# Optimization experiments

Hardware: AMD Instinct MI355X
Metric: run time of the kernel (lower is better)

## Reference

```python
import jax, jax.numpy as jnp
import numpy as np

B, S, D = 2, 1024, 1024
H, KV, HD = 16, 4, 64
E, K, F = 8, 2, 2048
EPS = 1e-6
THETA = 10000.0
LAYER = 0


def setup_inputs() -> dict:
    key = jax.random.key(0)
    ks = jax.random.split(key, 12)
    sc = 0.02
    return {
        "hidden_states": jax.random.normal(ks[0], (B, S, D), jnp.float32),
        "position_ids": jnp.broadcast_to(jnp.arange(S, dtype=jnp.int32), (B, S)),
        "gate_scores": jnp.zeros((1, B, S, E), jnp.float32),
        "ln1_w": jnp.ones((D,), jnp.float32),
        "ln2_w": jnp.ones((D,), jnp.float32),
        "wq": jax.random.normal(ks[1], (D, H * HD), jnp.float32) * sc,
        "wk": jax.random.normal(ks[2], (D, KV * HD), jnp.float32) * sc,
        "wv": jax.random.normal(ks[3], (D, KV * HD), jnp.float32) * sc,
        "wo": jax.random.normal(ks[4], (H * HD, D), jnp.float32) * sc,
        "gate_w": jax.random.normal(ks[5], (D, E), jnp.float32) * sc,
        "w1": jax.random.normal(ks[6], (E, D, F), jnp.float32) * sc,
        "w3": jax.random.normal(ks[7], (E, D, F), jnp.float32) * sc,
        "w2": jax.random.normal(ks[8], (E, F, D), jnp.float32) * sc,
    }


def rms_norm(x, w):
    var = jnp.mean(jnp.square(x), axis=-1, keepdims=True)
    return x * jax.lax.rsqrt(var + EPS) * w


def rotate_half(x):
    x1, x2 = jnp.split(x, 2, axis=-1)
    return jnp.concatenate([-x2, x1], axis=-1)


def apply_rope(q, k, position_ids):
    inv_freq = 1.0 / (THETA ** (jnp.arange(0, HD, 2, dtype=jnp.float32) / HD))
    freqs = position_ids.astype(jnp.float32)[..., None] * inv_freq  # [B,S,HD/2]
    emb = jnp.concatenate([freqs, freqs], axis=-1)  # [B,S,HD]
    cos = jnp.cos(emb)[:, :, None, :]
    sin = jnp.sin(emb)[:, :, None, :]
    q = q * cos + rotate_half(q) * sin
    k = k * cos + rotate_half(k) * sin
    return q, k


def attention(x, position_ids, wq, wk, wv, wo):
    q = (x @ wq).reshape(B, S, H, HD)
    k = (x @ wk).reshape(B, S, KV, HD)
    v = (x @ wv).reshape(B, S, KV, HD)
    q, k = apply_rope(q, k, position_ids)
    rep = H // KV
    k = jnp.repeat(k, rep, axis=2)  # [B,S,H,HD]
    v = jnp.repeat(v, rep, axis=2)
    scores = jnp.einsum("bqhd,bkhd->bhqk", q, k) / jnp.sqrt(jnp.float32(HD))
    causal = jnp.tril(jnp.ones((S, S), bool))
    scores = jnp.where(causal, scores, jnp.finfo(scores.dtype).min)
    p = jax.nn.softmax(scores, axis=-1)
    out = jnp.einsum("bhqk,bkhd->bqhd", p, v).reshape(B, S, H * HD)
    return out @ wo


def moe(x, gate_w, w1, w3, w2):
    xt = x.reshape(-1, D)  # [T,D]
    router_logits = xt @ gate_w  # [T,E]
    routing_weights = jax.nn.softmax(router_logits.astype(jnp.float32), axis=-1)
    routing_scores = routing_weights.reshape(B, S, E)
    top_w, top_e = jax.lax.top_k(routing_weights, K)  # [T,K]
    top_w = top_w / jnp.sum(top_w, axis=-1, keepdims=True)
    top_w = top_w.astype(xt.dtype)
    # combined per-(token,expert) weight; zero when not routed
    comb = jnp.sum(jax.nn.one_hot(top_e, E, dtype=xt.dtype) * top_w[..., None], axis=1)  # [T,E]
    # SwiGLU experts, dense-dispatch formulation (same math as gather/scatter)
    h = jax.nn.silu(jnp.einsum("td,edf->etf", xt, w1)) * jnp.einsum("td,edf->etf", xt, w3)
    y = jnp.einsum("etf,efd->etd", h, w2)  # [E,T,D]
    out = jnp.einsum("etd,te->td", y, comb)
    return out.reshape(B, S, D), routing_scores


def reference(hidden_states, position_ids, gate_scores, ln1_w, ln2_w, wq, wk, wv, wo, gate_w, w1, w3, w2):
    residual = hidden_states
    h = rms_norm(hidden_states, ln1_w)
    h = residual + attention(h, position_ids, wq, wk, wv, wo)
    residual = h
    hn = rms_norm(h, ln2_w)
    moe_out, routing_scores = moe(hn, gate_w, w1, w3, w2)
    h = residual + moe_out
    gate_scores = gate_scores.at[LAYER].set(routing_scores)
    return h, gate_scores
```

## Files before the change

kernel.cpp:

```cpp
#include <hip/hip_runtime.h>
#include <hip/hip_bf16.h>
#include <stdint.h>

using bf16 = __hip_bfloat16;
using bf16x8 = __attribute__((ext_vector_type(8))) __bf16;
using f32x4  = __attribute__((ext_vector_type(4))) float;

#define NTOK 2048
#define DIM 1024
#define NH 16
#define NKV 4
#define HDIM 64
#define NE 8
#define NF 2048
#define SEQ 1024
#define MAXR 5120
#define MAXTILES 40

__device__ __forceinline__ float b2f(unsigned short u){ unsigned v=((unsigned)u)<<16; float f; __builtin_memcpy(&f,&v,4); return f; }
__device__ __forceinline__ unsigned short f2b(float f){ bf16 h=__float2bfloat16(f); unsigned short u; __builtin_memcpy(&u,&h,2); return u; }

__global__ void k_zero_i32(int* p, int n){ int i=blockIdx.x*256+threadIdx.x; if(i<n) p[i]=0; }

__global__ __launch_bounds__(256) void k_transpose(const float* __restrict__ in, bf16* __restrict__ out, int R, int C){
  __shared__ float tile[32][33];
  int bx = blockIdx.x*32, by = blockIdx.y*32;
  size_t base = (size_t)blockIdx.z * R * C;
  int x = threadIdx.x, y0 = threadIdx.y;
  const float* src = in + base;
  bf16* dst = out + base;
#pragma unroll
  for (int i=0;i<4;i++){ int r = y0 + i*8; tile[r][x] = src[(size_t)(by+r)*C + bx + x]; }
  __syncthreads();
#pragma unroll
  for (int i=0;i<4;i++){ int c = y0 + i*8; dst[(size_t)(bx+c)*R + by + x] = __float2bfloat16(tile[x][c]); }
}

__global__ __launch_bounds__(256) void k_tbf(const bf16* __restrict__ in, bf16* __restrict__ out, int R, int C){
  __shared__ unsigned short tile[32][33];
  int bx = blockIdx.x*32, by = blockIdx.y*32;
  size_t base = (size_t)blockIdx.z * R * C;
  const unsigned short* src = (const unsigned short*)in + base;
  unsigned short* dst = (unsigned short*)out + base;
  int x = threadIdx.x, y0 = threadIdx.y;
#pragma unroll
  for (int i=0;i<4;i++){ int r = y0 + i*8; tile[r][x] = src[(size_t)(by+r)*C + bx + x]; }
  __syncthreads();
#pragma unroll
  for (int i=0;i<4;i++){ int c = y0 + i*8; dst[(size_t)(bx+c)*R + by + x] = tile[x][c]; }
}

__global__ __launch_bounds__(256) void k_rmsnorm(const float* __restrict__ x, const float* __restrict__ w, bf16* __restrict__ out){
  int row = blockIdx.x, t = threadIdx.x;
  const float4 v = ((const float4*)(x + (size_t)row*DIM))[t];
  float ss = v.x*v.x + v.y*v.y + v.z*v.z + v.w*v.w;
#pragma unroll
  for (int m=1;m<64;m<<=1) ss += __shfl_xor(ss, m);
  __shared__ float red[4];
  if ((t&63)==0) red[t>>6] = ss;
  __syncthreads();
  float tot = red[0]+red[1]+red[2]+red[3];
  float r = rsqrtf(tot * (1.0f/DIM) + 1e-6f);
  const float4 wv = ((const float4*)w)[t];
  ushort4 o;
  o.x = f2b(v.x*r*wv.x); o.y = f2b(v.y*r*wv.y); o.z = f2b(v.z*r*wv.z); o.w = f2b(v.w*r*wv.w);
  ((ushort4*)(out + (size_t)row*DIM))[t] = o;
}

#define BM 128
#define BN 128
#define BK 32

template<int MODE>
__global__ __launch_bounds__(256) void k_gemm(
    const bf16* __restrict__ A, const bf16* __restrict__ Bt,
    bf16* __restrict__ Cb, float* __restrict__ Cf, const float* __restrict__ resid,
    const int* __restrict__ tile_expert, const int* __restrict__ row_tok,
    const float* __restrict__ row_w, const int* __restrict__ row_slot,
    int N, int K)
{
  int tn = blockIdx.x, tm = blockIdx.y;
  int e = 0;
  if constexpr (MODE >= 2){ e = tile_expert[tm]; if (e < 0) return; }
  const bf16* Ablk = A + (size_t)tm*BM*K;
  const bf16* Bblk = Bt + ((MODE>=2) ? (size_t)e*N*K : (size_t)0) + (size_t)tn*BN*K;

  __shared__ bf16 lA[BM*BK];
  __shared__ bf16 lB[BN*BK];

  int t = threadIdx.x;
  int lane = t & 63, wave = t >> 6;
  int wr = wave >> 1, wc = wave & 1;
  int lr = lane & 15, lg = lane >> 4;

  int sr = t >> 2;
  int sk = (t & 3) * 8;

  f32x4 acc[4][4] = {};

  for (int k0 = 0; k0 < K; k0 += BK){
    bf16x8 va0 = *(const bf16x8*)(Ablk + (size_t)sr*K + k0 + sk);
    bf16x8 va1 = *(const bf16x8*)(Ablk + (size_t)(64+sr)*K + k0 + sk);
    bf16x8 vb0 = *(const bf16x8*)(Bblk + (size_t)sr*K + k0 + sk);
    bf16x8 vb1 = *(const bf16x8*)(Bblk + (size_t)(64+sr)*K + k0 + sk);
    __syncthreads();
    *(bf16x8*)(lA + t*8) = va0;
    *(bf16x8*)(lA + 2048 + t*8) = va1;
    *(bf16x8*)(lB + t*8) = vb0;
    *(bf16x8*)(lB + 2048 + t*8) = vb1;
    __syncthreads();
    bf16x8 af[4], bfv[4];
#pragma unroll
    for (int m=0;m<4;m++) af[m]  = *(const bf16x8*)(lA + (wr*64 + m*16 + lr)*BK + lg*8);
#pragma unroll
    for (int n=0;n<4;n++) bfv[n] = *(const bf16x8*)(lB + (wc*64 + n*16 + lr)*BK + lg*8);
#pragma unroll
    for (int m=0;m<4;m++)
#pragma unroll
      for (int n=0;n<4;n++)
        acc[m][n] = __builtin_amdgcn_mfma_f32_16x16x32_bf16(af[m], bfv[n], acc[m][n], 0, 0, 0);
  }

#pragma unroll
  for (int m=0;m<4;m++){
#pragma unroll
    for (int n=0;n<4;n++){
      int col = tn*BN + wc*64 + n*16 + lr;
#pragma unroll
      for (int j=0;j<4;j++){
        int row = tm*BM + wr*64 + m*16 + lg*4 + j;
        float v = acc[m][n][j];
        if constexpr (MODE==0 || MODE==2){
          Cb[(size_t)row*N + col] = __float2bfloat16(v);
        } else if constexpr (MODE==1){
          Cf[(size_t)row*N + col] = v + resid[(size_t)row*N + col];
        } else {
          int tok = row_tok[row];
          if (tok >= 0) Cf[((size_t)row_slot[row]*NTOK + tok)*DIM + col] = v * row_w[row];
        }
      }
    }
  }
}

__global__ __launch_bounds__(64) void k_rope(const bf16* __restrict__ qkv, const int* __restrict__ pos_ids,
    bf16* __restrict__ qr, bf16* __restrict__ kr, bf16* __restrict__ vr){
  int tk = blockIdx.x;
  int b = tk >> 10, s = tk & 1023;
  int d = threadIdx.x;
  float p = (float)pos_ids[tk];
  int i = d & 31;
  float freq = p * powf(10000.0f, -(float)(2*i)*(1.0f/HDIM));
  float sn, cs;
  sincosf(freq, &sn, &cs);
  const bf16* row = qkv + (size_t)tk*1536;
#pragma unroll
  for (int h=0; h<NH; h++){
    float x  = __bfloat162float(row[h*64 + d]);
    float xp = __bfloat162float(row[h*64 + ((d+32)&63)]);
    float rh = (d<32) ? -xp : xp;
    qr[(((size_t)(b*NH+h)*SEQ)+s)*HDIM + d] = __float2bfloat16(x*cs + rh*sn);
  }
#pragma unroll
  for (int h=0; h<NKV; h++){
    float x  = __bfloat162float(row[1024 + h*64 + d]);
    float xp = __bfloat162float(row[1024 + h*64 + ((d+32)&63)]);
    float rh = (d<32) ? -xp : xp;
    kr[(((size_t)(b*NKV+h)*SEQ)+s)*HDIM + d] = __float2bfloat16(x*cs + rh*sn);
    vr[(((size_t)(b*NKV+h)*SEQ)+s)*HDIM + d] = row[1280 + h*64 + d];
  }
}

__global__ __launch_bounds__(64) void k_attn_mfma(const bf16* __restrict__ qr, const bf16* __restrict__ kr,
    const bf16* __restrict__ vT, bf16* __restrict__ out){
  int qt = blockIdx.x, h = blockIdx.y, b = blockIdx.z;
  int lane = threadIdx.x;
  int g = lane >> 4, c = lane & 15;
  int kv = h >> 2;
  int qbase = qt*16;
  const bf16* Qb = qr + (((size_t)(b*NH+h)*SEQ) + qbase)*HDIM;
  const bf16* Kb = kr + ((size_t)(b*NKV+kv)*SEQ)*HDIM;
  const bf16* Vt = vT + ((size_t)(b*NKV+kv)*HDIM)*SEQ;

  bf16x8 qa[2];
  qa[0] = *(const bf16x8*)(Qb + (size_t)c*HDIM + g*8);
  qa[1] = *(const bf16x8*)(Qb + (size_t)c*HDIM + 32 + g*8);

  f32x4 acc[4] = {};
  float m[4], l[4];
#pragma unroll
  for (int j=0;j<4;j++){ m[j] = -1e30f; l[j] = 0.f; }

  __shared__ bf16 P[16][40];

  int kend = qbase + 15;
  for (int k0 = 0; k0 <= kend; k0 += 32){
    f32x4 s[2] = {};
#pragma unroll
    for (int cn=0;cn<2;cn++){
#pragma unroll
      for (int dk=0;dk<2;dk++){
        bf16x8 kb = *(const bf16x8*)(Kb + (size_t)(k0+cn*16+c)*HDIM + dk*32 + g*8);
        s[cn] = __builtin_amdgcn_mfma_f32_16x16x32_bf16(qa[dk], kb, s[cn], 0, 0, 0);
      }
    }
    float sv[2][4];
    bool boundary = (k0 + 31 > qbase);
#pragma unroll
    for (int cn=0;cn<2;cn++){
#pragma unroll
      for (int j=0;j<4;j++){
        float v = s[cn][j] * 0.125f;
        if (boundary){
          int cg = k0 + cn*16 + c, rg = qbase + g*4 + j;
          if (cg > rg) v = -1e30f;
        }
        sv[cn][j] = v;
      }
    }
#pragma unroll
    for (int j=0;j<4;j++){
      float rmax = fmaxf(sv[0][j], sv[1][j]);
#pragma unroll
      for (int mk=1;mk<16;mk<<=1) rmax = fmaxf(rmax, __shfl_xor(rmax, mk));
      float mn = fmaxf(m[j], rmax);
      float corr = __expf(m[j] - mn);
      m[j] = mn;
      float p0 = __expf(sv[0][j] - mn);
      float p1 = __expf(sv[1][j] - mn);
      float rs = p0 + p1;
#pragma unroll
      for (int mk=1;mk<16;mk<<=1) rs += __shfl_xor(rs, mk);
      l[j] = l[j]*corr + rs;
#pragma unroll
      for (int db=0;db<4;db++) acc[db][j] *= corr;
      P[g*4+j][c]      = __float2bfloat16(p0);
      P[g*4+j][16+c]   = __float2bfloat16(p1);
    }
    __syncthreads();
    bf16x8 pa = *(const bf16x8*)(&P[c][g*8]);
#pragma unroll
    for (int db=0;db<4;db++){
      bf16x8 vb = *(const bf16x8*)(Vt + (size_t)(db*16+c)*SEQ + k0 + g*8);
      acc[db] = __builtin_amdgcn_mfma_f32_16x16x32_bf16(pa, vb, acc[db], 0, 0, 0);
    }
    __syncthreads();
  }
#pragma unroll
  for (int j=0;j<4;j++){
    float inv = 1.f / l[j];
    size_t rowoff = (size_t)(b*SEQ + qbase + g*4 + j)*1024 + h*64;
#pragma unroll
    for (int db=0;db<4;db++)
      out[rowoff + db*16 + c] = __float2bfloat16(acc[db][j] * inv);
  }
}

__global__ __launch_bounds__(64) void k_router(const float* __restrict__ h1, const float* __restrict__ ln2w,
    const float* __restrict__ gw, float* __restrict__ scores,
    int* __restrict__ top_e, float* __restrict__ top_w, int* __restrict__ cnt){
  int tk = blockIdx.x, lane = threadIdx.x;
  const float* xr = h1 + (size_t)tk*DIM;
  const float4* x4 = (const float4*)xr;
  float4 xv[4];
  float ss = 0.f;
#pragma unroll
  for (int i=0;i<4;i++){
    xv[i] = x4[lane*4+i];
    ss += xv[i].x*xv[i].x + xv[i].y*xv[i].y + xv[i].z*xv[i].z + xv[i].w*xv[i].w;
  }
#pragma unroll
  for (int mm=1;mm<64;mm<<=1) ss += __shfl_xor(ss, mm);
  float r = rsqrtf(ss*(1.0f/DIM) + 1e-6f);
  float acc[8] = {0,0,0,0,0,0,0,0};
#pragma unroll
  for (int i=0;i<16;i++){
    int d = lane*16 + i;
    float xd = ((const float*)xv)[i];
    float xn = xd * r * ln2w[d];
    const float* g = gw + (size_t)d*NE;
#pragma unroll
    for (int e=0;e<8;e++) acc[e] += xn * g[e];
  }
#pragma unroll
  for (int e=0;e<8;e++){
#pragma unroll
    for (int mm=1;mm<64;mm<<=1) acc[e] += __shfl_xor(acc[e], mm);
  }
  float mx = acc[0];
#pragma unroll
  for (int e=1;e<8;e++) mx = fmaxf(mx, acc[e]);
  float w[8]; float se = 0.f;
#pragma unroll
  for (int e=0;e<8;e++){ w[e] = expf(acc[e]-mx); se += w[e]; }
  float inv = 1.f/se;
#pragma unroll
  for (int e=0;e<8;e++) w[e] *= inv;
  if (lane < 8) scores[(size_t)tk*NE + lane] = w[lane];
  if (lane == 0){
    int e1=0; float m1=w[0];
#pragma unroll
    for (int i=1;i<8;i++) if (w[i] > m1){ m1=w[i]; e1=i; }
    int e2=-1; float m2=-1.f;
#pragma unroll
    for (int i=0;i<8;i++) if (i!=e1 && w[i] > m2){ m2=w[i]; e2=i; }
    float s12 = m1 + m2;
    top_e[2*tk] = e1;   top_w[2*tk]   = m1/s12;
    top_e[2*tk+1] = e2; top_w[2*tk+1] = m2/s12;
    atomicAdd(&cnt[e1], 1); atomicAdd(&cnt[e2], 1);
  }
}

__global__ __launch_bounds__(256) void k_offsets(const int* __restrict__ cnt, int* __restrict__ seg_off,
    int* __restrict__ tile_expert, int* __restrict__ row_tok){
  int t = threadIdx.x;
  for (int i=t;i<MAXR;i+=256) row_tok[i] = -1;
  for (int i=t;i<MAXTILES;i+=256) tile_expert[i] = -1;
  __syncthreads();
  if (t == 0){
    int off = 0;
    for (int e=0;e<NE;e++){
      seg_off[e] = off;
      int nt = (cnt[e] + 127) >> 7;
      for (int i=0;i<nt;i++) tile_expert[(off>>7)+i] = e;
      off += nt << 7;
    }
  }
}

__global__ __launch_bounds__(256) void k_scatter(const int* __restrict__ top_e, const float* __restrict__ top_w,
    const int* __restrict__ seg_off, int* __restrict__ cnt2,
    int* __restrict__ row_tok, float* __restrict__ row_w, int* __restrict__ row_slot){
  int tkn = blockIdx.x*256 + threadIdx.x;
  if (tkn >= NTOK) return;
#pragma unroll
  for (int k=0;k<2;k++){
    int e = top_e[2*tkn+k];
    int p = atomicAdd(&cnt2[e], 1);
    int r = seg_off[e] + p;
    row_tok[r] = tkn; row_w[r] = top_w[2*tkn+k]; row_slot[r] = k;
  }
}

__global__ __launch_bounds__(256) void k_gather(const int* __restrict__ row_tok, const bf16* __restrict__ xn,
    bf16* __restrict__ Xg){
  int r = blockIdx.x, t = threadIdx.x;
  int tok = row_tok[r];
  ushort4* dst = (ushort4*)(Xg + (size_t)r*DIM) + t;
  if (tok < 0){ ushort4 z; z.x=0; z.y=0; z.z=0; z.w=0; *dst = z; }
  else *dst = ((const ushort4*)(xn + (size_t)tok*DIM))[t];
}

__global__ __launch_bounds__(256) void k_silumul(const bf16* __restrict__ a, const bf16* __restrict__ b, bf16* __restrict__ o){
  size_t i = (size_t)blockIdx.x*256 + threadIdx.x;
  ushort4 ua = ((const ushort4*)a)[i];
  ushort4 ub = ((const ushort4*)b)[i];
  ushort4 uo;
  { float fa=b2f(ua.x), fb=b2f(ub.x); uo.x = f2b(fa/(1.f+__expf(-fa))*fb); }
  { float fa=b2f(ua.y), fb=b2f(ub.y); uo.y = f2b(fa/(1.f+__expf(-fa))*fb); }
  { float fa=b2f(ua.z), fb=b2f(ub.z); uo.z = f2b(fa/(1.f+__expf(-fa))*fb); }
  { float fa=b2f(ua.w), fb=b2f(ub.w); uo.w = f2b(fa/(1.f+__expf(-fa))*fb); }
  ((ushort4*)o)[i] = uo;
}

__global__ __launch_bounds__(256) void k_final(const float* __restrict__ h1, const float* __restrict__ ybuf, float* __restrict__ out){
  size_t i = (size_t)blockIdx.x*256 + threadIdx.x;
  float4 a  = ((const float4*)h1)[i];
  float4 b0 = ((const float4*)ybuf)[i];
  float4 b1 = ((const float4*)(ybuf + (size_t)NTOK*DIM))[i];
  float4 r;
  r.x = a.x+b0.x+b1.x; r.y = a.y+b0.y+b1.y; r.z = a.z+b0.z+b1.z; r.w = a.w+b0.w+b1.w;
  ((float4*)out)[i] = r;
}

extern "C" void kernel_launch(void* const* d_in, const int* in_sizes, int n_in,
                              void* d_out, int out_size, void* d_ws, size_t ws_size,
                              hipStream_t stream){
  const float* hidden = (const float*)d_in[0];
  const int*   pos    = (const int*)d_in[1];
  const float* ln1    = (const float*)d_in[3];
  const float* ln2    = (const float*)d_in[4];
  const float* wq     = (const float*)d_in[5];
  const float* wk     = (const float*)d_in[6];
  const float* wv     = (const float*)d_in[7];
  const float* wo     = (const float*)d_in[8];
  const float* gw     = (const float*)d_in[9];
  const float* w1     = (const float*)d_in[10];
  const float* w3     = (const float*)d_in[11];
  const float* w2     = (const float*)d_in[12];
  float* out1 = (float*)d_out;
  float* out2 = out1 + (size_t)NTOK*DIM;

  char* p = (char*)d_ws;
  auto take = [&](size_t bytes){ void* r = (void*)p; p += (bytes + 255) & ~(size_t)255; return r; };
  bf16* wqkvT = (bf16*)take((size_t)1536*1024*2);
  bf16* woT   = (bf16*)take((size_t)1024*1024*2);
  bf16* w1T   = (bf16*)take((size_t)NE*NF*DIM*2);
  bf16* w3T   = (bf16*)take((size_t)NE*NF*DIM*2);
  bf16* w2T   = (bf16*)take((size_t)NE*DIM*NF*2);
  float* h1   = (float*)take((size_t)NTOK*DIM*4);
  bf16* xn2   = (bf16*)take((size_t)NTOK*DIM*2);
  int*  cnt   = (int*)take(64);
  int*  cnt2  = cnt + 8;
  int*  seg_off     = (int*)take(64);
  int*  tile_expert = (int*)take(MAXTILES*4);
  int*  top_e  = (int*)take((size_t)NTOK*2*4);
  float* top_w = (float*)take((size_t)NTOK*2*4);
  int*  row_tok  = (int*)take((size_t)MAXR*4);
  float* row_w   = (float*)take((size_t)MAXR*4);
  int*  row_slot = (int*)take((size_t)MAXR*4);
  bf16* Xg    = (bf16*)take((size_t)MAXR*DIM*2);
  bf16* h1buf = (bf16*)take((size_t)MAXR*NF*2);
  bf16* h3buf = (bf16*)take((size_t)MAXR*NF*2);
  bf16* hbuf  = (bf16*)take((size_t)MAXR*NF*2);
  char* ra = (char*)Xg;
  bf16* xn1 = (bf16*)ra;       ra += (size_t)NTOK*DIM*2;
  bf16* qkv = (bf16*)ra;       ra += (size_t)NTOK*1536*2;
  bf16* qr  = (bf16*)ra;       ra += (size_t)NTOK*DIM*2;
  bf16* krp = (bf16*)ra;       ra += (size_t)NTOK*NKV*HDIM*2;
  bf16* vrp = (bf16*)ra;       ra += (size_t)NTOK*NKV*HDIM*2;
  bf16* vTp = (bf16*)ra;       ra += (size_t)NTOK*NKV*HDIM*2;
  bf16* attn_out = (bf16*)ra;  ra += (size_t)NTOK*DIM*2;
  float* ybuf = (float*)h1buf;

  k_zero_i32<<<dim3(1), dim3(256), 0, stream>>>(cnt, 16);
  k_transpose<<<dim3(32,32,1), dim3(32,8), 0, stream>>>(wq, wqkvT, 1024, 1024);
  k_transpose<<<dim3(8,32,1),  dim3(32,8), 0, stream>>>(wk, wqkvT + (size_t)1024*1024, 1024, 256);
  k_transpose<<<dim3(8,32,1),  dim3(32,8), 0, stream>>>(wv, wqkvT + (size_t)1280*1024, 1024, 256);
  k_transpose<<<dim3(32,32,1), dim3(32,8), 0, stream>>>(wo, woT, 1024, 1024);
  k_transpose<<<dim3(NF/32, DIM/32, NE), dim3(32,8), 0, stream>>>(w1, w1T, DIM, NF);
  k_transpose<<<dim3(NF/32, DIM/32, NE), dim3(32,8), 0, stream>>>(w3, w3T, DIM, NF);
  k_transpose<<<dim3(DIM/32, NF/32, NE), dim3(32,8), 0, stream>>>(w2, w2T, NF, DIM);
  k_rmsnorm<<<dim3(NTOK), dim3(256), 0, stream>>>(hidden, ln1, xn1);
  k_gemm<0><<<dim3(1536/BN, NTOK/BM), dim3(256), 0, stream>>>(xn1, wqkvT, qkv, nullptr, nullptr, nullptr, nullptr, nullptr, nullptr, 1536, 1024);
  k_rope<<<dim3(NTOK), dim3(64), 0, stream>>>(qkv, pos, qr, krp, vrp);
  k_tbf<<<dim3(HDIM/32, SEQ/32, 2*NKV), dim3(32,8), 0, stream>>>(vrp, vTp, SEQ, HDIM);
  k_attn_mfma<<<dim3(SEQ/16, NH, 2), dim3(64), 0, stream>>>(qr, krp, vTp, attn_out);
  k_gemm<1><<<dim3(DIM/BN, NTOK/BM), dim3(256), 0, stream>>>(attn_out, woT, nullptr, h1, hidden, nullptr, nullptr, nullptr, nullptr, DIM, 1024);
  k_rmsnorm<<<dim3(NTOK), dim3(256), 0, stream>>>(h1, ln2, xn2);
  k_router<<<dim3(NTOK), dim3(64), 0, stream>>>(h1, ln2, gw, out2, top_e, top_w, cnt);
  k_offsets<<<dim3(1), dim3(256), 0, stream>>>(cnt, seg_off, tile_expert, row_tok);
  k_scatter<<<dim3(NTOK/256), dim3(256), 0, stream>>>(top_e, top_w, seg_off, cnt2, row_tok, row_w, row_slot);
  k_gather<<<dim3(MAXR), dim3(256), 0, stream>>>(row_tok, xn2, Xg);
  k_gemm<2><<<dim3(NF/BN, MAXTILES), dim3(256), 0, stream>>>(Xg, w1T, h1buf, nullptr, nullptr, tile_expert, nullptr, nullptr, nullptr, NF, DIM);
  k_gemm<2><<<dim3(NF/BN, MAXTILES), dim3(256), 0, stream>>>(Xg, w3T, h3buf, nullptr, nullptr, tile_expert, nullptr, nullptr, nullptr, NF, DIM);
  k_silumul<<<dim3((unsigned)((size_t)MAXR*NF/4/256)), dim3(256), 0, stream>>>(h1buf, h3buf, hbuf);
  k_gemm<3><<<dim3(DIM/BN, MAXTILES), dim3(256), 0, stream>>>(hbuf, w2T, nullptr, ybuf, nullptr, tile_expert, row_tok, row_w, row_slot, DIM, NF);
  k_final<<<dim3(NTOK*DIM/4/256), dim3(256), 0, stream>>>(h1, ybuf, out1);
}
```

Baseline: 621.9 us.

## Load GEMM tiles directly to LDS and fuse w1/w3 expert GEMMs

The GEMM staging now uses global_load_lds so tiles go from global memory straight into LDS, skipping the register round-trip, and the per-wave row mapping is changed to match. The w1 and w3 expert weights are transposed into one interleaved buffer per expert so a single grouped GEMM with doubled N produces both projections. The SiLU-multiply kernel reads both halves from each row of that buffer. This saves a launch and one read of the gathered activations, but the direct-to-LDS path needs its layout to line up with the MFMA fragment reads.

```diff
diff --git a/kernel.cpp b/kernel.cpp
--- a/kernel.cpp
+++ b/kernel.cpp
@@ -20,15 +20,21 @@
 __device__ __forceinline__ float b2f(unsigned short u){ unsigned v=((unsigned)u)<<16; float f; __builtin_memcpy(&f,&v,4); return f; }
 __device__ __forceinline__ unsigned short f2b(float f){ bf16 h=__float2bfloat16(f); unsigned short u; __builtin_memcpy(&u,&h,2); return u; }
 
+typedef __attribute__((address_space(3))) unsigned int lds_u32;
+typedef const __attribute__((address_space(1))) unsigned int glb_u32;
+__device__ __forceinline__ void lds16(const void* g, void* l){
+  __builtin_amdgcn_global_load_lds((glb_u32*)g, (lds_u32*)l, 16, 0, 0);
+}
+
 __global__ void k_zero_i32(int* p, int n){ int i=blockIdx.x*256+threadIdx.x; if(i<n) p[i]=0; }
 
-__global__ __launch_bounds__(256) void k_transpose(const float* __restrict__ in, bf16* __restrict__ out, int R, int C){
+__global__ __launch_bounds__(256) void k_transpose(const float* __restrict__ in, bf16* __restrict__ out,
+    int R, int C, size_t inz, size_t outz){
   __shared__ float tile[32][33];
   int bx = blockIdx.x*32, by = blockIdx.y*32;
-  size_t base = (size_t)blockIdx.z * R * C;
+  const float* src = in + (size_t)blockIdx.z * inz;
+  bf16* dst = out + (size_t)blockIdx.z * outz;
   int x = threadIdx.x, y0 = threadIdx.y;
-  const float* src = in + base;
-  bf16* dst = out + base;
 #pragma unroll
   for (int i=0;i<4;i++){ int r = y0 + i*8; tile[r][x] = src[(size_t)(by+r)*C + bx + x]; }
   __syncthreads();
@@ -93,21 +99,17 @@
   int wr = wave >> 1, wc = wave & 1;
   int lr = lane & 15, lg = lane >> 4;
 
-  int sr = t >> 2;
-  int sk = (t & 3) * 8;
+  int srow = wave*32 + (lane >> 2);
+  int scol = (lane & 3) * 8;
 
   f32x4 acc[4][4] = {};
 
   for (int k0 = 0; k0 < K; k0 += BK){
-    bf16x8 va0 = *(const bf16x8*)(Ablk + (size_t)sr*K + k0 + sk);
-    bf16x8 va1 = *(const bf16x8*)(Ablk + (size_t)(64+sr)*K + k0 + sk);
-    bf16x8 vb0 = *(const bf16x8*)(Bblk + (size_t)sr*K + k0 + sk);
-    bf16x8 vb1 = *(const bf16x8*)(Bblk + (size_t)(64+sr)*K + k0 + sk);
     __syncthreads();
-    *(bf16x8*)(lA + t*8) = va0;
-    *(bf16x8*)(lA + 2048 + t*8) = va1;
-    *(bf16x8*)(lB + t*8) = vb0;
-    *(bf16x8*)(lB + 2048 + t*8) = vb1;
+    lds16(Ablk + (size_t)srow*K        + k0 + scol, lA + wave*1024);
+    lds16(Ablk + (size_t)(srow+16)*K   + k0 + scol, lA + wave*1024 + 512);
+    lds16(Bblk + (size_t)srow*K        + k0 + scol, lB + wave*1024);
+    lds16(Bblk + (size_t)(srow+16)*K   + k0 + scol, lB + wave*1024 + 512);
     __syncthreads();
     bf16x8 af[4], bfv[4];
 #pragma unroll
@@ -351,16 +353,19 @@
   else *dst = ((const ushort4*)(xn + (size_t)tok*DIM))[t];
 }
 
-__global__ __launch_bounds__(256) void k_silumul(const bf16* __restrict__ a, const bf16* __restrict__ b, bf16* __restrict__ o){
+__global__ __launch_bounds__(256) void k_silumul(const bf16* __restrict__ h13, bf16* __restrict__ o){
   size_t i = (size_t)blockIdx.x*256 + threadIdx.x;
-  ushort4 ua = ((const ushort4*)a)[i];
-  ushort4 ub = ((const ushort4*)b)[i];
+  size_t r = i >> 9;
+  int fq = (int)(i & 511);
+  const bf16* rowp = h13 + r*(2*NF);
+  ushort4 ua = ((const ushort4*)rowp)[fq];
+  ushort4 ub = ((const ushort4*)(rowp + NF))[fq];
   ushort4 uo;
   { float fa=b2f(ua.x), fb=b2f(ub.x); uo.x = f2b(fa/(1.f+__expf(-fa))*fb); }
   { float fa=b2f(ua.y), fb=b2f(ub.y); uo.y = f2b(fa/(1.f+__expf(-fa))*fb); }
   { float fa=b2f(ua.z), fb=b2f(ub.z); uo.z = f2b(fa/(1.f+__expf(-fa))*fb); }
   { float fa=b2f(ua.w), fb=b2f(ub.w); uo.w = f2b(fa/(1.f+__expf(-fa))*fb); }
-  ((ushort4*)o)[i] = uo;
+  ((ushort4*)(o))[i] = uo;
 }
 
 __global__ __launch_bounds__(256) void k_final(const float* __restrict__ h1, const float* __restrict__ ybuf, float* __restrict__ out){
@@ -395,8 +400,7 @@
   auto take = [&](size_t bytes){ void* r = (void*)p; p += (bytes + 255) & ~(size_t)255; return r; };
   bf16* wqkvT = (bf16*)take((size_t)1536*1024*2);
   bf16* woT   = (bf16*)take((size_t)1024*1024*2);
-  bf16* w1T   = (bf16*)take((size_t)NE*NF*DIM*2);
-  bf16* w3T   = (bf16*)take((size_t)NE*NF*DIM*2);
+  bf16* w13T  = (bf16*)take((size_t)NE*2*NF*DIM*2);
   bf16* w2T   = (bf16*)take((size_t)NE*DIM*NF*2);
   float* h1   = (float*)take((size_t)NTOK*DIM*4);
   bf16* xn2   = (bf16*)take((size_t)NTOK*DIM*2);
@@ -409,10 +413,9 @@
   int*  row_tok  = (int*)take((size_t)MAXR*4);
   float* row_w   = (float*)take((size_t)MAXR*4);
   int*  row_slot = (int*)take((size_t)MAXR*4);
-  bf16* Xg    = (bf16*)take((size_t)MAXR*DIM*2);
-  bf16* h1buf = (bf16*)take((size_t)MAXR*NF*2);
-  bf16* h3buf = (bf16*)take((size_t)MAXR*NF*2);
-  bf16* hbuf  = (bf16*)take((size_t)MAXR*NF*2);
+  bf16* Xg     = (bf16*)take((size_t)MAXR*DIM*2);
+  bf16* h13buf = (bf16*)take((size_t)MAXR*2*NF*2);
+  bf16* hbuf   = (bf16*)take((size_t)MAXR*NF*2);
   char* ra = (char*)Xg;
   bf16* xn1 = (bf16*)ra;       ra += (size_t)NTOK*DIM*2;
   bf16* qkv = (bf16*)ra;       ra += (size_t)NTOK*1536*2;
@@ -421,16 +424,16 @@
   bf16* vrp = (bf16*)ra;       ra += (size_t)NTOK*NKV*HDIM*2;
   bf16* vTp = (bf16*)ra;       ra += (size_t)NTOK*NKV*HDIM*2;
   bf16* attn_out = (bf16*)ra;  ra += (size_t)NTOK*DIM*2;
-  float* ybuf = (float*)h1buf;
+  float* ybuf = (float*)h13buf;
 
   k_zero_i32<<<dim3(1), dim3(256), 0, stream>>>(cnt, 16);
-  k_transpose<<<dim3(32,32,1), dim3(32,8), 0, stream>>>(wq, wqkvT, 1024, 1024);
-  k_transpose<<<dim3(8,32,1),  dim3(32,8), 0, stream>>>(wk, wqkvT + (size_t)1024*1024, 1024, 256);
-  k_transpose<<<dim3(8,32,1),  dim3(32,8), 0, stream>>>(wv, wqkvT + (size_t)1280*1024, 1024, 256);
-  k_transpose<<<dim3(32,32,1), dim3(32,8), 0, stream>>>(wo, woT, 1024, 1024);
-  k_transpose<<<dim3(NF/32, DIM/32, NE), dim3(32,8), 0, stream>>>(w1, w1T, DIM, NF);
-  k_transpose<<<dim3(NF/32, DIM/32, NE), dim3(32,8), 0, stream>>>(w3, w3T, DIM, NF);
-  k_transpose<<<dim3(DIM/32, NF/32, NE), dim3(32,8), 0, stream>>>(w2, w2T, NF, DIM);
+  k_transpose<<<dim3(32,32,1), dim3(32,8), 0, stream>>>(wq, wqkvT, 1024, 1024, (size_t)1024*1024, (size_t)1024*1024);
+  k_transpose<<<dim3(8,32,1),  dim3(32,8), 0, stream>>>(wk, wqkvT + (size_t)1024*1024, 1024, 256, (size_t)1024*256, (size_t)1024*256);
+  k_transpose<<<dim3(8,32,1),  dim3(32,8), 0, stream>>>(wv, wqkvT + (size_t)1280*1024, 1024, 256, (size_t)1024*256, (size_t)1024*256);
+  k_transpose<<<dim3(32,32,1), dim3(32,8), 0, stream>>>(wo, woT, 1024, 1024, (size_t)1024*1024, (size_t)1024*1024);
+  k_transpose<<<dim3(NF/32, DIM/32, NE), dim3(32,8), 0, stream>>>(w1, w13T, DIM, NF, (size_t)DIM*NF, (size_t)2*NF*DIM);
+  k_transpose<<<dim3(NF/32, DIM/32, NE), dim3(32,8), 0, stream>>>(w3, w13T + (size_t)NF*DIM, DIM, NF, (size_t)DIM*NF, (size_t)2*NF*DIM);
+  k_transpose<<<dim3(DIM/32, NF/32, NE), dim3(32,8), 0, stream>>>(w2, w2T, NF, DIM, (size_t)NF*DIM, (size_t)NF*DIM);
   k_rmsnorm<<<dim3(NTOK), dim3(256), 0, stream>>>(hidden, ln1, xn1);
   k_gemm<0><<<dim3(1536/BN, NTOK/BM), dim3(256), 0, stream>>>(xn1, wqkvT, qkv, nullptr, nullptr, nullptr, nullptr, nullptr, nullptr, 1536, 1024);
   k_rope<<<dim3(NTOK), dim3(64), 0, stream>>>(qkv, pos, qr, krp, vrp);
@@ -442,9 +445,8 @@
   k_offsets<<<dim3(1), dim3(256), 0, stream>>>(cnt, seg_off, tile_expert, row_tok);
   k_scatter<<<dim3(NTOK/256), dim3(256), 0, stream>>>(top_e, top_w, seg_off, cnt2, row_tok, row_w, row_slot);
   k_gather<<<dim3(MAXR), dim3(256), 0, stream>>>(row_tok, xn2, Xg);
-  k_gemm<2><<<dim3(NF/BN, MAXTILES), dim3(256), 0, stream>>>(Xg, w1T, h1buf, nullptr, nullptr, tile_expert, nullptr, nullptr, nullptr, NF, DIM);
-  k_gemm<2><<<dim3(NF/BN, MAXTILES), dim3(256), 0, stream>>>(Xg, w3T, h3buf, nullptr, nullptr, tile_expert, nullptr, nullptr, nullptr, NF, DIM);
-  k_silumul<<<dim3((unsigned)((size_t)MAXR*NF/4/256)), dim3(256), 0, stream>>>(h1buf, h3buf, hbuf);
+  k_gemm<2><<<dim3(2*NF/BN, MAXTILES), dim3(256), 0, stream>>>(Xg, w13T, h13buf, nullptr, nullptr, tile_expert, nullptr, nullptr, nullptr, 2*NF, DIM);
+  k_silumul<<<dim3((unsigned)((size_t)MAXR*NF/4/256)), dim3(256), 0, stream>>>(h13buf, hbuf);
   k_gemm<3><<<dim3(DIM/BN, MAXTILES), dim3(256), 0, stream>>>(hbuf, w2T, nullptr, ybuf, nullptr, tile_expert, row_tok, row_w, row_slot, DIM, NF);
   k_final<<<dim3(NTOK*DIM/4/256), dim3(256), 0, stream>>>(h1, ybuf, out1);
 }
```

Measured after the change: 617.0 us. Within noise of the previous version (-0.8%).
